# Kernel optimization log

Hardware: AMD Instinct MI355X
Metric: run time of the kernel (lower is better)

## Reference

```python
import jax, jax.numpy as jnp
import numpy as np

B, S, E, H = 2, 2048, 1024, 16
D = E // H  # head_dim = 64


def setup_inputs() -> dict:
    key = jax.random.key(0)
    ks = jax.random.split(key, 6)
    scale = 1.0 / np.sqrt(E)
    x = jax.random.normal(ks[0], (B, S, E), dtype=jnp.float32)
    mask = jnp.ones((B, S), dtype=jnp.int32)
    Wqkv = jax.random.normal(ks[1], (E, 3 * E), dtype=jnp.float32) * scale
    bqkv = jax.random.normal(ks[2], (3 * E,), dtype=jnp.float32) * 0.01
    Wout = jax.random.normal(ks[3], (E, E), dtype=jnp.float32) * scale
    bout = jax.random.normal(ks[4], (E,), dtype=jnp.float32) * 0.01
    return {"x": x, "mask": mask, "Wqkv": Wqkv, "bqkv": bqkv, "Wout": Wout, "bout": bout}


def reference(x, mask, Wqkv, bqkv, Wout, bout):
    Bn, Sn, En = x.shape
    qkv = x @ Wqkv + bqkv                      # [B,S,3E]
    qkv = qkv.reshape(Bn, Sn, 3, H, D)
    qkv = jnp.transpose(qkv, (2, 0, 3, 1, 4))  # [3,B,H,S,D]
    q, k, v = qkv[0], qkv[1], qkv[2]
    scores = jnp.einsum('bhqd,bhkd->bhqk', q, k) / np.sqrt(D).astype(np.float32)
    m = mask[:, None, None, :]                 # [B,1,1,S]
    scores = jnp.where(m == 0, jnp.float32(-jnp.inf), scores)
    attn = jax.nn.softmax(scores, axis=-1)
    out = jnp.einsum('bhqk,bhkd->bhqd', attn, v)  # [B,H,S,D]
    out = jnp.transpose(out, (0, 2, 1, 3)).reshape(Bn, Sn, En)
    return out @ Wout + bout
```

## Files before the change

### kernel.cpp

```cpp
#include <hip/hip_runtime.h>


typedef __attribute__((ext_vector_type(8))) short short8;
typedef __attribute__((ext_vector_type(4))) short short4b;
typedef __attribute__((ext_vector_type(4))) float floatx4;
typedef __attribute__((ext_vector_type(16))) float floatx16;
typedef unsigned short ushort_t;

static __device__ __forceinline__ ushort_t f2bf(float f) {
    unsigned u = __float_as_uint(f);
    u += 0x7fffu + ((u >> 16) & 1u);
    return (ushort_t)(u >> 16);
}
static __device__ __forceinline__ float bf2f(ushort_t h) {
    return __uint_as_float(((unsigned)h) << 16);
}
#if __has_builtin(__builtin_amdgcn_cvt_pk_bf16_f32)
typedef __attribute__((ext_vector_type(2))) __bf16 bf16x2_t;
static __device__ __forceinline__ unsigned pack2bf(float a, float b) {
    bf16x2_t r = __builtin_amdgcn_cvt_pk_bf16_f32(a, b);
    return __builtin_bit_cast(unsigned, r);
}
#else
static __device__ __forceinline__ unsigned pack2bf(float a, float b) {
    return (unsigned)f2bf(a) | ((unsigned)f2bf(b) << 16);
}
#endif
static __device__ __forceinline__ float hexp2(float x) {
    return __builtin_amdgcn_exp2f(x);
}
static __device__ __forceinline__ void gload16(const void* g, void* l) {
    __builtin_amdgcn_global_load_lds(
        (const __attribute__((address_space(1))) unsigned int*)g,
        (__attribute__((address_space(3))) unsigned int*)l, 16, 0, 0);
}

#if __has_builtin(__builtin_amdgcn_permlane32_swap)
typedef __attribute__((ext_vector_type(2))) unsigned uint2v_t;
static __device__ __forceinline__ void plswap(unsigned x, unsigned y,
                                              unsigned& o0, unsigned& o1) {
    uint2v_t r = __builtin_amdgcn_permlane32_swap(x, y, false, false);
    o0 = r.x; o1 = r.y;
}
#else
static __device__ __forceinline__ void plswap(unsigned x, unsigned y,
                                              unsigned& o0, unsigned& o1) {
    int l = (int)(threadIdx.x & 63);
    bool hi = l >= 32;
    unsigned xsw = (unsigned)__shfl((int)x, l ^ 32);
    unsigned ysw = (unsigned)__shfl((int)y, l ^ 32);
    o0 = hi ? ysw : x;
    o1 = hi ? y : xsw;
}
#endif

__global__ __launch_bounds__(256) void prep(
    const float* __restrict__ x, ushort_t* __restrict__ xb,
    const float* __restrict__ Wqkv, ushort_t* __restrict__ wqT,
    const float* __restrict__ Wout, ushort_t* __restrict__ woT,
    const int* __restrict__ mask, float* __restrict__ maddg)
{
    __shared__ float tile[32][33];
    const int bk = blockIdx.x;
    const int t = threadIdx.x;
    if (bk < 4096) {
        int i = bk * 256 + t;
        float4 v = ((const float4*)x)[i];
        uint2 o;
        o.x = pack2bf(v.x, v.y);
        o.y = pack2bf(v.z, v.w);
        ((uint2*)xb)[i] = o;
        return;
    }
    if (bk < 8192) {
        const float* W; ushort_t* WT; int K, N, id;
        if (bk < 7168) { W = Wqkv; WT = wqT; K = 1024; N = 3072; id = bk - 4096;
                         int nb = (id % 96) * 32, kb = (id / 96) * 32;
                         const int r = t >> 3, c4 = (t & 7) * 4;
                         float4 v = *(const float4*)&W[(size_t)(kb + r) * N + nb + c4];
                         tile[r][c4+0]=v.x; tile[r][c4+1]=v.y; tile[r][c4+2]=v.z; tile[r][c4+3]=v.w;
                         __syncthreads();
                         uint2 o;
                         o.x = pack2bf(tile[c4+0][r], tile[c4+1][r]);
                         o.y = pack2bf(tile[c4+2][r], tile[c4+3][r]);
                         ((uint2*)WT)[((size_t)(nb + r) * K + kb + c4) >> 2] = o;
        } else {         W = Wout; WT = woT; K = 1024; N = 1024; id = bk - 7168;
                         int nb = (id % 32) * 32, kb = (id / 32) * 32;
                         const int r = t >> 3, c4 = (t & 7) * 4;
                         float4 v = *(const float4*)&W[(size_t)(kb + r) * N + nb + c4];
                         tile[r][c4+0]=v.x; tile[r][c4+1]=v.y; tile[r][c4+2]=v.z; tile[r][c4+3]=v.w;
                         __syncthreads();
                         uint2 o;
                         o.x = pack2bf(tile[c4+0][r], tile[c4+1][r]);
                         o.y = pack2bf(tile[c4+2][r], tile[c4+3][r]);
                         ((uint2*)WT)[((size_t)(nb + r) * K + kb + c4) >> 2] = o;
        }
        return;
    }
    {
        int i = (bk - 8192) * 256 + t;
        maddg[i] = (mask[i] ? 0.f : -1e30f) - 24.0f;
    }
}

__global__ __launch_bounds__(256, 3) void gemm_qkv(
    const ushort_t* __restrict__ A, const ushort_t* __restrict__ B,
    const float* __restrict__ bias, ushort_t* __restrict__ qkvb,
    ushort_t* __restrict__ vtg)
{
    const int K = 1024;
    __shared__ ushort_t Ah[128][32], Bh[128][32];
    __shared__ ushort_t Tb[64][136];
    const int bn = blockIdx.x * 128, bm = blockIdx.y * 128;
    const int t = threadIdx.x, w = t >> 6, lane = t & 63;
    const int l15 = lane & 15, quad = lane >> 4;
    const int wm = w >> 1, wn = w & 1;

    const int srow = w * 32 + (lane >> 2);
    const int skp  = (lane & 3) ^ ((lane >> 2) & 3);
    const int scol = skp * 8;
    const ushort_t* ga = A + (size_t)(bm + srow) * K + scol;
    const ushort_t* gb = B + (size_t)(bn + srow) * K + scol;
    const size_t rstep = (size_t)16 * K;
    const int fcol = ((quad ^ (l15 & 3)) * 8);

    floatx4 acc[4][4];
    #pragma unroll
    for (int mt = 0; mt < 4; ++mt)
        #pragma unroll
        for (int nt = 0; nt < 4; ++nt) acc[mt][nt] = (floatx4){0.f, 0.f, 0.f, 0.f};

    for (int k0 = 0; k0 < K; k0 += 32) {
        #pragma unroll
        for (int i = 0; i < 2; ++i) {
            gload16(ga + i * rstep + k0, &Ah[w * 32 + i * 16][0]);
            gload16(gb + i * rstep + k0, &Bh[w * 32 + i * 16][0]);
        }
        __syncthreads();
        short8 ah[4], bh[4];
        #pragma unroll
        for (int x = 0; x < 4; ++x) {
            ah[x] = *(const short8*)&Ah[wm * 64 + x * 16 + l15][fcol];
            bh[x] = *(const short8*)&Bh[wn * 64 + x * 16 + l15][fcol];
        }
        #pragma unroll
        for (int mt = 0; mt < 4; ++mt)
            #pragma unroll
            for (int nt = 0; nt < 4; ++nt)
                acc[mt][nt] = __builtin_amdgcn_mfma_f32_16x16x32_bf16(ah[mt], bh[nt], acc[mt][nt], 0, 0, 0);
        __syncthreads();
    }

    if (bn < 2048) {
        #pragma unroll
        for (int mt = 0; mt < 4; ++mt)
            #pragma unroll
            for (int r = 0; r < 4; ++r) {
                size_t row = (size_t)(bm + wm * 64 + mt * 16 + quad * 4 + r) * 2048;
                #pragma unroll
                for (int nt = 0; nt < 4; ++nt) {
                    int col = bn + wn * 64 + nt * 16 + l15;
                    qkvb[row + col] = f2bf(acc[mt][nt][r] + bias[col]);
                }
            }
    } else {
        const int h0 = (bn - 2048) >> 6;
        const int b  = bm >> 11, s0 = bm & 2047;
        #pragma unroll
        for (int hh = 0; hh < 2; ++hh) {
            if (wn == hh) {
                #pragma unroll
                for (int mt = 0; mt < 4; ++mt)
                    #pragma unroll
                    for (int nt = 0; nt < 4; ++nt) {
                        int d = nt * 16 + l15;
                        int sb = wm * 64 + mt * 16 + quad * 4;
                        float bv = bias[bn + hh * 64 + nt * 16 + l15];
                        uint2 pk;
                        pk.x = pack2bf(acc[mt][nt][0] + bv, acc[mt][nt][1] + bv);
                        pk.y = pack2bf(acc[mt][nt][2] + bv, acc[mt][nt][3] + bv);
                        *(uint2*)&Tb[d][sb] = pk;
                    }
            }
            __syncthreads();
            ushort_t* vbase = vtg + ((size_t)((b * 16 + h0 + hh) * 64)) * 2048 + s0;
            #pragma unroll
            for (int it = 0; it < 4; ++it) {
                int idx = t + it * 256;
                int d = idx >> 4, ch = idx & 15;
                uint4 v = *(const uint4*)&Tb[d][ch * 8];
                *(uint4*)&vbase[(size_t)d * 2048 + ch * 8] = v;
            }
            __syncthreads();
        }
    }
}

__global__ __launch_bounds__(256, 3) void gemm_bf16_f32_64(
    const ushort_t* __restrict__ A, const ushort_t* __restrict__ B,
    const float* __restrict__ bias, float* __restrict__ C,
    int M, int N, int K)
{
    __shared__ ushort_t Ah[64][32], Bh[128][32];
    const int bn = blockIdx.x * 128, bm = blockIdx.y * 64;
    const int t = threadIdx.x, w = t >> 6, lane = t & 63;
    const int l15 = lane & 15, quad = lane >> 4;
    const int wm = w >> 1, wn = w & 1;

    const int srow = w * 16 + (lane >> 2);
    const int skp  = (lane & 3) ^ ((lane >> 2) & 3);
    const int scol = skp * 8;
    const ushort_t* ga  = A + (size_t)(bm + srow) * K + scol;
    const ushort_t* gb0 = B + (size_t)(bn + srow) * K + scol;
    const ushort_t* gb1 = B + (size_t)(bn + 64 + srow) * K + scol;
    const int fcol = ((quad ^ (l15 & 3)) * 8);

    floatx4 acc[2][4];
    #pragma unroll
    for (int mt = 0; mt < 2; ++mt)
        #pragma unroll
        for (int nt = 0; nt < 4; ++nt) acc[mt][nt] = (floatx4){0.f, 0.f, 0.f, 0.f};

    for (int k0 = 0; k0 < K; k0 += 32) {
        gload16(ga  + k0, &Ah[w * 16][0]);
        gload16(gb0 + k0, &Bh[w * 16][0]);
        gload16(gb1 + k0, &Bh[64 + w * 16][0]);
        __syncthreads();
        short8 ah[2], bh[4];
        #pragma unroll
        for (int x = 0; x < 2; ++x)
            ah[x] = *(const short8*)&Ah[wm * 32 + x * 16 + l15][fcol];
        #pragma unroll
        for (int x = 0; x < 4; ++x)
            bh[x] = *(const short8*)&Bh[wn * 64 + x * 16 + l15][fcol];
        #pragma unroll
        for (int mt = 0; mt < 2; ++mt)
            #pragma unroll
            for (int nt = 0; nt < 4; ++nt)
                acc[mt][nt] = __builtin_amdgcn_mfma_f32_16x16x32_bf16(ah[mt], bh[nt], acc[mt][nt], 0, 0, 0);
        __syncthreads();
    }
    #pragma unroll
    for (int mt = 0; mt < 2; ++mt)
        #pragma unroll
        for (int r = 0; r < 4; ++r) {
            size_t row = (size_t)(bm + wm * 32 + mt * 16 + quad * 4 + r) * N;
            #pragma unroll
            for (int nt = 0; nt < 4; ++nt) {
                int col = bn + wn * 64 + nt * 16 + l15;
                C[row + col] = acc[mt][nt][r] + bias[col];
            }
        }
}

__global__ __launch_bounds__(512)
__attribute__((amdgpu_waves_per_eu(4, 4)))
void flash_v12(
    const ushort_t* __restrict__ qkv, const ushort_t* __restrict__ vtg,
    const float* __restrict__ maddg, ushort_t* __restrict__ attn)
{
    __shared__ __align__(16) ushort_t Ks[2][2][64][64];
    __shared__ __align__(16) ushort_t Vt[2][2][64][64];

    const int blk = blockIdx.x;
    const int xcd = blk & 7, rr = blk >> 3;
    const int qi = rr & 15, g = xcd + 8 * (rr >> 4);
    const int b = g >> 4, h = g & 15, q0 = qi * 128;

    const int t = threadIdx.x, wave = t >> 6, lane = t & 63;
    const int half = wave >> 2, wsub = wave & 3;
    const int l31 = lane & 31, hi = lane >> 5, l7 = lane & 7;
    const size_t bS = (size_t)b * 2048;
    const float c1 = 0.125f * 1.44269504088896340736f;

    short8 qf[4];
    {
        int q = q0 + wsub * 32 + l31;
        const ushort_t* qp = qkv + (bS + q) * 2048 + h * 64 + hi * 8;
        #pragma unroll
        for (int ks = 0; ks < 4; ++ks)
            qf[ks] = *(const short8*)(qp + ks * 16);
    }

    const int srow  = wsub * 16 + (lane >> 3);
    const int schnk = ((lane & 7) ^ ((lane >> 3) & 7)) * 8;
    const ushort_t* gK = qkv + (bS + half * 1024 + srow) * 2048 + 1024 + h * 64 + schnk;
    const ushort_t* gV = vtg + ((size_t)(b * 16 + h) * 64 + srow) * 2048 + half * 1024 + schnk;
    const float* gM = maddg + b * 2048 + half * 1024;

    gload16(gK,            &Ks[half][0][wsub * 16][0]);
    gload16(gK + 8 * 2048, &Ks[half][0][wsub * 16 + 8][0]);
    gload16(gV,            &Vt[half][0][wsub * 16][0]);
    gload16(gV + 8 * 2048, &Vt[half][0][wsub * 16 + 8][0]);
    __syncthreads();

    floatx16 outacc[2] = {};
    float lsum = 0.f;

    int cur = 0;
    for (int kt = 0; kt < 16; ++kt) {
        const int k0 = kt * 64;
        if (kt + 1 < 16) {
            const int kn = (kt + 1) * 64;
            const int nb = cur ^ 1;
            gload16(gK + (size_t)kn * 2048,       &Ks[half][nb][wsub * 16][0]);
            gload16(gK + (size_t)(kn + 8) * 2048, &Ks[half][nb][wsub * 16 + 8][0]);
            gload16(gV + kn,                      &Vt[half][nb][wsub * 16][0]);
            gload16(gV + kn + 8 * 2048,           &Vt[half][nb][wsub * 16 + 8][0]);
        }

        unsigned W[2][4][2];
        #pragma unroll
        for (int t32 = 0; t32 < 2; ++t32) {
            floatx16 sc = {};
            __builtin_amdgcn_s_setprio(1);
            #pragma unroll
            for (int ks = 0; ks < 4; ++ks) {
                const int ch = ((2 * ks + hi) ^ l7) * 8;
                short8 ka = *(const short8*)&Ks[half][cur][t32 * 32 + l31][ch];
                sc = __builtin_amdgcn_mfma_f32_32x32x16_bf16(ka, qf[ks], sc, 0, 0, 0);
            }
            __builtin_amdgcn_s_setprio(0);
            #pragma unroll
            for (int gr = 0; gr < 4; ++gr) {
                float4 m4 = *(const float4*)&gM[k0 + t32 * 32 + gr * 8 + hi * 4];
                float p0 = hexp2(fmaf(sc[gr * 4 + 0], c1, m4.x));
                float p1 = hexp2(fmaf(sc[gr * 4 + 1], c1, m4.y));
                float p2 = hexp2(fmaf(sc[gr * 4 + 2], c1, m4.z));
                float p3 = hexp2(fmaf(sc[gr * 4 + 3], c1, m4.w));
                lsum += (p0 + p1) + (p2 + p3);
                W[t32][gr][0] = pack2bf(p0, p1);
                W[t32][gr][1] = pack2bf(p2, p3);
            }
        }

        #pragma unroll
        for (int ks2 = 0; ks2 < 4; ++ks2) {
            const int t32 = ks2 >> 1;
            const int ae  = (ks2 & 1) * 2;
            uint4 u;
            plswap(W[t32][ae][0], W[t32][ae + 1][0], u.x, u.z);
            plswap(W[t32][ae][1], W[t32][ae + 1][1], u.y, u.w);
            short8 pb = __builtin_bit_cast(short8, u);
            const int ch = ((2 * ks2 + hi) ^ l7) * 8;
            __builtin_amdgcn_s_setprio(1);
            #pragma unroll
            for (int dt = 0; dt < 2; ++dt) {
                short8 va = *(const short8*)&Vt[half][cur][dt * 32 + l31][ch];
                outacc[dt] = __builtin_amdgcn_mfma_f32_32x32x16_bf16(va, pb, outacc[dt], 0, 0, 0);
            }
            __builtin_amdgcn_s_setprio(0);
        }
        __syncthreads();
        cur ^= 1;
    }

    lsum += __shfl_xor(lsum, 32);

    float* Obuf = (float*)&Ks[0][0][0][0];
    float* Lbuf = (float*)&Vt[0][0][0][0];

    if (half == 1) {
        #pragma unroll
        for (int dt = 0; dt < 2; ++dt)
            #pragma unroll
            for (int i = 0; i < 16; ++i)
                Obuf[(wsub * 64 + lane) * 32 + ((dt * 16 + i) ^ l31)] = outacc[dt][i];
        Lbuf[wsub * 32 + l31] = lsum;
    }
    __syncthreads();
    if (half == 0) {
        float inv = 1.f / (lsum + Lbuf[wsub * 32 + l31]);
        int q = q0 + wsub * 32 + l31;
        ushort_t* orow = attn + (bS + q) * 1024 + h * 64;
        #pragma unroll
        for (int dt = 0; dt < 2; ++dt) {
            float o[16];
            #pragma unroll
            for (int i = 0; i < 16; ++i)
                o[i] = outacc[dt][i] + Obuf[(wsub * 64 + lane) * 32 + ((dt * 16 + i) ^ l31)];
            #pragma unroll
            for (int gr = 0; gr < 4; ++gr) {
                uint2 pk;
                pk.x = pack2bf(o[gr * 4 + 0] * inv, o[gr * 4 + 1] * inv);
                pk.y = pack2bf(o[gr * 4 + 2] * inv, o[gr * 4 + 3] * inv);
                *(uint2*)&orow[dt * 32 + gr * 8 + hi * 4] = pk;
            }
        }
    }
}

extern "C" void kernel_launch(void* const* d_in, const int* in_sizes, int n_in,
                              void* d_out, int out_size, void* d_ws, size_t ws_size,
                              hipStream_t stream) {
    const float* x    = (const float*)d_in[0];
    const int*   mask = (const int*)  d_in[1];
    const float* Wqkv = (const float*)d_in[2];
    const float* bqkv = (const float*)d_in[3];
    const float* Wout = (const float*)d_in[4];
    const float* bout = (const float*)d_in[5];
    float* out = (float*)d_out;

    char* ws = (char*)d_ws;
    ushort_t* xb    = (ushort_t*)(ws);
    ushort_t* wqT   = (ushort_t*)(ws + 8388608);
    ushort_t* qkvb  = (ushort_t*)(ws + 14680064);
    ushort_t* vtg   = (ushort_t*)(ws + 31457280);
    ushort_t* attnb = (ushort_t*)(ws + 39845888);
    ushort_t* woT   = (ushort_t*)(ws + 48234496);
    float*    maddg = (float*)   (ws + 50331648);

    const int M = 4096, E = 1024, N3 = 3072;

    prep<<<dim3(8208), dim3(256), 0, stream>>>(
        x, xb, Wqkv, wqT, Wout, woT, mask, maddg);

    gemm_qkv<<<dim3(N3 / 128, M / 128), dim3(256), 0, stream>>>(
        xb, wqT, bqkv, qkvb, vtg);

    flash_v12<<<dim3(512), dim3(512), 0, stream>>>(qkvb, vtg, maddg, attnb);

    gemm_bf16_f32_64<<<dim3(E / 128, M / 64), dim3(256), 0, stream>>>(
        attnb, woT, bout, out, M, E, E);
}
```

Baseline: 197.0 us.

## Software-pipeline attention loop: overlap next-tile QK softmax with current PV

Restructures the flash attention loop so the QK^T MFMAs and exp/softmax for tile kt+1 run in the same iteration as the PV MFMAs for tile kt. K is now prefetched two tiles ahead and V one tile ahead, and the packed probabilities are carried between iterations in registers. The aim is to hide exp/VALU latency behind matrix work and break the serial dependency within each iteration. The cost is roughly 16 extra live VGPRs for the next-tile probabilities under a fixed waves-per-EU budget, which risks spills, plus an extra prologue step and sync.

```diff
diff --git a/kernel.cpp b/kernel.cpp
--- a/kernel.cpp
+++ b/kernel.cpp
@@ -255,7 +255,7 @@
 
 __global__ __launch_bounds__(512)
 __attribute__((amdgpu_waves_per_eu(4, 4)))
-void flash_v12(
+void flash_v13(
     const ushort_t* __restrict__ qkv, const ushort_t* __restrict__ vtg,
     const float* __restrict__ maddg, ushort_t* __restrict__ attn)
 {
@@ -288,28 +288,21 @@
     const ushort_t* gV = vtg + ((size_t)(b * 16 + h) * 64 + srow) * 2048 + half * 1024 + schnk;
     const float* gM = maddg + b * 2048 + half * 1024;
 
-    gload16(gK,            &Ks[half][0][wsub * 16][0]);
-    gload16(gK + 8 * 2048, &Ks[half][0][wsub * 16 + 8][0]);
-    gload16(gV,            &Vt[half][0][wsub * 16][0]);
-    gload16(gV + 8 * 2048, &Vt[half][0][wsub * 16 + 8][0]);
-    __syncthreads();
+    auto stageK = [&](int buf, int kkt) {
+        const ushort_t* p = gK + (size_t)(kkt * 64) * 2048;
+        gload16(p,            &Ks[half][buf][wsub * 16][0]);
+        gload16(p + 8 * 2048, &Ks[half][buf][wsub * 16 + 8][0]);
+    };
+    auto stageV = [&](int buf, int kkt) {
+        gload16(gV + kkt * 64,            &Vt[half][buf][wsub * 16][0]);
+        gload16(gV + kkt * 64 + 8 * 2048, &Vt[half][buf][wsub * 16 + 8][0]);
+    };
 
     floatx16 outacc[2] = {};
     float lsum = 0.f;
 
-    int cur = 0;
-    for (int kt = 0; kt < 16; ++kt) {
-        const int k0 = kt * 64;
-        if (kt + 1 < 16) {
-            const int kn = (kt + 1) * 64;
-            const int nb = cur ^ 1;
-            gload16(gK + (size_t)kn * 2048,       &Ks[half][nb][wsub * 16][0]);
-            gload16(gK + (size_t)(kn + 8) * 2048, &Ks[half][nb][wsub * 16 + 8][0]);
-            gload16(gV + kn,                      &Vt[half][nb][wsub * 16][0]);
-            gload16(gV + kn + 8 * 2048,           &Vt[half][nb][wsub * 16 + 8][0]);
-        }
-
-        unsigned W[2][4][2];
+    auto QKSM = [&](int kkt, int kb, unsigned (&Wd)[2][4][2]) {
+        const int k0 = kkt * 64;
         #pragma unroll
         for (int t32 = 0; t32 < 2; ++t32) {
             floatx16 sc = {};
@@ -317,7 +310,7 @@
             #pragma unroll
             for (int ks = 0; ks < 4; ++ks) {
                 const int ch = ((2 * ks + hi) ^ l7) * 8;
-                short8 ka = *(const short8*)&Ks[half][cur][t32 * 32 + l31][ch];
+                short8 ka = *(const short8*)&Ks[half][kb][t32 * 32 + l31][ch];
                 sc = __builtin_amdgcn_mfma_f32_32x32x16_bf16(ka, qf[ks], sc, 0, 0, 0);
             }
             __builtin_amdgcn_s_setprio(0);
@@ -329,30 +322,55 @@
                 float p2 = hexp2(fmaf(sc[gr * 4 + 2], c1, m4.z));
                 float p3 = hexp2(fmaf(sc[gr * 4 + 3], c1, m4.w));
                 lsum += (p0 + p1) + (p2 + p3);
-                W[t32][gr][0] = pack2bf(p0, p1);
-                W[t32][gr][1] = pack2bf(p2, p3);
-            }
-        }
-
+                Wd[t32][gr][0] = pack2bf(p0, p1);
+                Wd[t32][gr][1] = pack2bf(p2, p3);
+            }
+        }
+    };
+    auto PV = [&](int vb, unsigned (&Wd)[2][4][2]) {
         #pragma unroll
         for (int ks2 = 0; ks2 < 4; ++ks2) {
             const int t32 = ks2 >> 1;
             const int ae  = (ks2 & 1) * 2;
             uint4 u;
-            plswap(W[t32][ae][0], W[t32][ae + 1][0], u.x, u.z);
-            plswap(W[t32][ae][1], W[t32][ae + 1][1], u.y, u.w);
+            plswap(Wd[t32][ae][0], Wd[t32][ae + 1][0], u.x, u.z);
+            plswap(Wd[t32][ae][1], Wd[t32][ae + 1][1], u.y, u.w);
             short8 pb = __builtin_bit_cast(short8, u);
             const int ch = ((2 * ks2 + hi) ^ l7) * 8;
             __builtin_amdgcn_s_setprio(1);
             #pragma unroll
             for (int dt = 0; dt < 2; ++dt) {
-                short8 va = *(const short8*)&Vt[half][cur][dt * 32 + l31][ch];
+                short8 va = *(const short8*)&Vt[half][vb][dt * 32 + l31][ch];
                 outacc[dt] = __builtin_amdgcn_mfma_f32_32x32x16_bf16(va, pb, outacc[dt], 0, 0, 0);
             }
             __builtin_amdgcn_s_setprio(0);
         }
+    };
+
+    stageK(0, 0);
+    stageK(1, 1);
+    stageV(0, 0);
+    __syncthreads();
+    unsigned Wc[2][4][2];
+    QKSM(0, 0, Wc);
+    __syncthreads();
+
+    for (int kt = 0; kt < 16; ++kt) {
+        if (kt + 2 < 16) stageK(kt & 1, kt + 2);
+        if (kt + 1 < 16) stageV((kt + 1) & 1, kt + 1);
+        unsigned Wn[2][4][2];
+        if (kt + 1 < 16) QKSM(kt + 1, (kt + 1) & 1, Wn);
+        PV(kt & 1, Wc);
         __syncthreads();
-        cur ^= 1;
+        if (kt + 1 < 16) {
+            #pragma unroll
+            for (int i = 0; i < 2; ++i)
+                #pragma unroll
+                for (int j = 0; j < 4; ++j) {
+                    Wc[i][j][0] = Wn[i][j][0];
+                    Wc[i][j][1] = Wn[i][j][1];
+                }
+        }
     }
 
     lsum += __shfl_xor(lsum, 32);
@@ -418,7 +436,7 @@
     gemm_qkv<<<dim3(N3 / 128, M / 128), dim3(256), 0, stream>>>(
         xb, wqT, bqkv, qkvb, vtg);
 
-    flash_v12<<<dim3(512), dim3(512), 0, stream>>>(qkvb, vtg, maddg, attnb);
+    flash_v13<<<dim3(512), dim3(512), 0, stream>>>(qkvb, vtg, maddg, attnb);
 
     gemm_bf16_f32_64<<<dim3(E / 128, M / 64), dim3(256), 0, stream>>>(
         attnb, woT, bout, out, M, E, E);
```

Result: slower. 205.7 us (+4.4%).
